# Optimization experiments

Hardware: AMD Instinct MI355X
Metric: run time of the kernel (lower is better)

Reference implementation:

```python
import jax, jax.numpy as jnp
import numpy as np

DIM = 512
HEADS = 8
DIM_HEAD = 32
INNER = HEADS * DIM_HEAD  # 256
B, N = 2, 2048
EPS = 1e-5


def setup_inputs() -> dict:
    key = jax.random.key(0)
    ks = jax.random.split(key, 6)
    x = jax.random.normal(ks[0], (B, N, DIM), dtype=jnp.float32)
    rel_pos_bias = jax.random.normal(ks[1], (HEADS, N, N), dtype=jnp.float32)
    ln_scale = jnp.ones((DIM,), dtype=jnp.float32)
    w_qkv = jax.random.normal(ks[2], (DIM, INNER * 3), dtype=jnp.float32) / np.sqrt(DIM)
    w_out = jax.random.normal(ks[3], (INNER, DIM), dtype=jnp.float32) / np.sqrt(INNER)
    b_out = jnp.zeros((DIM,), dtype=jnp.float32)
    return {"x": x, "rel_pos_bias": rel_pos_bias, "ln_scale": ln_scale,
            "w_qkv": w_qkv, "w_out": w_out, "b_out": b_out}


def reference(x, rel_pos_bias, ln_scale, w_qkv, w_out, b_out):
    scale = DIM_HEAD ** -0.5
    # LayerNorm (no bias), eps=1e-5
    mu = jnp.mean(x, axis=-1, keepdims=True)
    var = jnp.mean(jnp.square(x - mu), axis=-1, keepdims=True)
    xn = (x - mu) * jax.lax.rsqrt(var + EPS) * ln_scale
    # fused QKV projection, no bias
    qkv = xn @ w_qkv  # [b, n, 3*inner]
    q, k, v = jnp.split(qkv, 3, axis=-1)
    def to_heads(t):
        b, n, _ = t.shape
        return t.reshape(b, n, HEADS, DIM_HEAD).transpose(0, 2, 1, 3)  # b h n d
    q, k, v = map(to_heads, (q, k, v))
    q = q * scale
    sim = jnp.einsum('bhid,bhjd->bhij', q, k)
    sim = sim + rel_pos_bias  # (h,n,n) broadcasts over batch
    attn = jax.nn.softmax(sim, axis=-1)
    o = jnp.einsum('bhij,bhjd->bhid', attn, v)
    o = o.transpose(0, 2, 1, 3).reshape(x.shape[0], x.shape[1], INNER)  # b n (h d)
    return o @ w_out + b_out
```

## Files before the change

### kernel.cpp

```cpp
#include <hip/hip_runtime.h>
#include <hip/hip_bf16.h>
#include <cstdint>

#define NB 2
#define NSEQ 2048
#define NDIM 512
#define NHEAD 8
#define DHEAD 32
#define NINNER 256
#define NQKV 768
#define LNEPS 1e-5f
#define QSCALE 0.17677669529663687f

typedef short short8 __attribute__((ext_vector_type(8)));
typedef float f32x4 __attribute__((ext_vector_type(4)));
typedef unsigned short u16;
typedef unsigned int u32;

__device__ __forceinline__ f32x4 mfma16(short8 a, short8 b, f32x4 c) {
    return __builtin_amdgcn_mfma_f32_16x16x32_bf16(a, b, c, 0, 0, 0);
}

__device__ __forceinline__ u16 f2bf(float a) {
    union { float f; u32 u; } x; x.f = a;
    u32 r = x.u + 0x7fffu + ((x.u >> 16) & 1u);
    return (u16)(r >> 16);
}
__device__ __forceinline__ float bf2f(u16 h) {
    union { float f; u32 u; } x; x.u = ((u32)h) << 16; return x.f;
}
__device__ __forceinline__ void split2(float a, u16& hi, u16& lo) {
    hi = f2bf(a);
    lo = f2bf(a - bf2f(hi));
}

__global__ __launch_bounds__(256) void ln_kernel(
    const float* __restrict__ x, const float* __restrict__ gamma,
    u32* __restrict__ xn_hi, u32* __restrict__ xn_lo)
{
    const int row = blockIdx.x;
    const int t = threadIdx.x;
    const float2 v = ((const float2*)(x + (size_t)row * NDIM))[t];
    float s1 = v.x + v.y;
    float s2 = v.x * v.x + v.y * v.y;
    #pragma unroll
    for (int off = 32; off >= 1; off >>= 1) {
        s1 += __shfl_down(s1, off);
        s2 += __shfl_down(s2, off);
    }
    __shared__ float a1[4], a2[4];
    if ((t & 63) == 0) { a1[t >> 6] = s1; a2[t >> 6] = s2; }
    __syncthreads();
    const float ts1 = a1[0] + a1[1] + a1[2] + a1[3];
    const float ts2 = a2[0] + a2[1] + a2[2] + a2[3];
    const float mu = ts1 * (1.0f / NDIM);
    const float var = ts2 * (1.0f / NDIM) - mu * mu;
    const float rs = rsqrtf(var + LNEPS);
    const float2 g = ((const float2*)gamma)[t];
    const float xn0 = (v.x - mu) * rs * g.x;
    const float xn1 = (v.y - mu) * rs * g.y;
    u16 h0, l0, h1, l1;
    split2(xn0, h0, l0);
    split2(xn1, h1, l1);
    xn_hi[(size_t)row * (NDIM / 2) + t] = (u32)h0 | ((u32)h1 << 16);
    xn_lo[(size_t)row * (NDIM / 2) + t] = (u32)l0 | ((u32)l1 << 16);
}

__global__ __launch_bounds__(256) void wsplit_kernel(
    const float* __restrict__ w, u16* __restrict__ tT_hi, u16* __restrict__ tT_lo,
    int K, int Ncols)
{
    const int idx = blockIdx.x * 256 + threadIdx.x;
    const int k = idx / Ncols;
    const int n = idx - k * Ncols;
    u16 hh, ll;
    split2(w[idx], hh, ll);
    tT_hi[(size_t)n * K + k] = hh;
    tT_lo[(size_t)n * K + k] = ll;
}

__global__ __launch_bounds__(256, 4) void qkv_kernel(
    const u16* __restrict__ xn_hi, const u16* __restrict__ xn_lo,
    const u16* __restrict__ wT_hi, const u16* __restrict__ wT_lo,
    u16* __restrict__ q_hi, u16* __restrict__ q_lo,
    u16* __restrict__ k_hi, u16* __restrict__ k_lo,
    u16* __restrict__ vt_hi)
{
    const int t = threadIdx.x;
    const int wave = t >> 6, lane = t & 63;
    const int lrow = lane & 15, lquad = lane >> 4;
    const int rowBase = blockIdx.x * 64;
    const int colBase = blockIdx.y * 64;
    const int wm = (wave >> 1) * 32;
    const int wn = (wave & 1) * 32;
    const int kf = lquad * 8;
    const size_t arow0 = (size_t)(rowBase + wm + lrow) * NDIM;
    const size_t arow1 = (size_t)(rowBase + wm + 16 + lrow) * NDIM;
    const size_t brow0 = (size_t)(colBase + wn + lrow) * NDIM;
    const size_t brow1 = (size_t)(colBase + wn + 16 + lrow) * NDIM;
    const f32x4 zero = {0.f, 0.f, 0.f, 0.f};
    f32x4 acc00 = zero, acc01 = zero, acc10 = zero, acc11 = zero;

    for (int k0 = 0; k0 < NDIM; k0 += 32) {
        const short8 a0h = *(const short8*)(xn_hi + arow0 + k0 + kf);
        const short8 a0l = *(const short8*)(xn_lo + arow0 + k0 + kf);
        const short8 a1h = *(const short8*)(xn_hi + arow1 + k0 + kf);
        const short8 a1l = *(const short8*)(xn_lo + arow1 + k0 + kf);
        const short8 b0h = *(const short8*)(wT_hi + brow0 + k0 + kf);
        const short8 b0l = *(const short8*)(wT_lo + brow0 + k0 + kf);
        const short8 b1h = *(const short8*)(wT_hi + brow1 + k0 + kf);
        const short8 b1l = *(const short8*)(wT_lo + brow1 + k0 + kf);
        acc00 = mfma16(a0h, b0h, acc00); acc00 = mfma16(a0h, b0l, acc00); acc00 = mfma16(a0l, b0h, acc00);
        acc01 = mfma16(a0h, b1h, acc01); acc01 = mfma16(a0h, b1l, acc01); acc01 = mfma16(a0l, b1h, acc01);
        acc10 = mfma16(a1h, b0h, acc10); acc10 = mfma16(a1h, b0l, acc10); acc10 = mfma16(a1l, b0h, acc10);
        acc11 = mfma16(a1h, b1h, acc11); acc11 = mfma16(a1h, b1l, acc11); acc11 = mfma16(a1l, b1h, acc11);
    }

    #pragma unroll
    for (int mi = 0; mi < 2; mi++) {
        #pragma unroll
        for (int ni = 0; ni < 2; ni++) {
            f32x4 acc = (mi == 0) ? ((ni == 0) ? acc00 : acc01)
                                  : ((ni == 0) ? acc10 : acc11);
            #pragma unroll
            for (int r = 0; r < 4; r++) {
                const int grow = rowBase + wm + mi * 16 + lquad * 4 + r;
                const int gcol = colBase + wn + ni * 16 + lrow;
                const float v = acc[r];
                const int bidx = grow >> 11;
                const int n = grow & (NSEQ - 1);
                const int sec = gcol >> 8;
                const int idx = gcol & 255;
                const int head = idx >> 5, d = idx & 31;
                const int bh = bidx * NHEAD + head;
                if (sec == 0) {
                    u16 hh, ll;
                    split2(v * QSCALE, hh, ll);
                    const size_t a = ((size_t)bh * NSEQ + n) * DHEAD + d;
                    q_hi[a] = hh; q_lo[a] = ll;
                } else if (sec == 1) {
                    u16 hh, ll;
                    split2(v, hh, ll);
                    const size_t a = ((size_t)bh * NSEQ + n) * DHEAD + d;
                    k_hi[a] = hh; k_lo[a] = ll;
                } else {
                    const size_t a = ((size_t)bh * DHEAD + d) * NSEQ + n;
                    vt_hi[a] = f2bf(v);
                }
            }
        }
    }
}

__global__ __launch_bounds__(256, 6) void attn_kernel(
    const u16* __restrict__ q_hi, const u16* __restrict__ q_lo,
    const u16* __restrict__ k_hi, const u16* __restrict__ k_lo,
    const u16* __restrict__ vt_hi,
    const float* __restrict__ bias,
    u16* __restrict__ o_hi, u16* __restrict__ o_lo)
{
    __shared__ __align__(16) u16 Ph[4][16][40];
    __shared__ __align__(16) float cA[4][64][4];
    __shared__ __align__(16) float cB[4][64][4];
    __shared__ float cl[4][16];
    const int t = threadIdx.x;
    const int wave = t >> 6, lane = t & 63;
    const int lrow = lane & 15, lquad = lane >> 4;
    const int bh = blockIdx.y;
    const int head = bh & (NHEAD - 1);
    const int qb = blockIdx.x * 16;
    const size_t qkbase = (size_t)bh * NSEQ * DHEAD;
    const short8 qh = *(const short8*)(q_hi + qkbase + (size_t)(qb + lrow) * DHEAD + lquad * 8);
    const short8 ql = *(const short8*)(q_lo + qkbase + (size_t)(qb + lrow) * DHEAD + lquad * 8);
    const f32x4 zero = {0.f, 0.f, 0.f, 0.f};
    f32x4 accA = zero, accB = zero;
    float lp[4] = {0.f, 0.f, 0.f, 0.f};
    const float* biasrow = bias + (size_t)head * NSEQ * NSEQ + (size_t)(qb + lquad * 4) * NSEQ + lrow;
    const size_t vbase = (size_t)bh * DHEAD * NSEQ;
    const int ktbase = wave * 512;

    for (int i = 0; i < 16; i++) {
        const int kt = ktbase + i * 32;
        const short8 kh0 = *(const short8*)(k_hi + qkbase + (size_t)(kt + lrow) * DHEAD + lquad * 8);
        const short8 kl0 = *(const short8*)(k_lo + qkbase + (size_t)(kt + lrow) * DHEAD + lquad * 8);
        const short8 kh1 = *(const short8*)(k_hi + qkbase + (size_t)(kt + 16 + lrow) * DHEAD + lquad * 8);
        const short8 kl1 = *(const short8*)(k_lo + qkbase + (size_t)(kt + 16 + lrow) * DHEAD + lquad * 8);
        f32x4 s0 = zero, s1 = zero;
        s0 = mfma16(qh, kh0, s0); s0 = mfma16(qh, kl0, s0); s0 = mfma16(ql, kh0, s0);
        s1 = mfma16(qh, kh1, s1); s1 = mfma16(qh, kl1, s1); s1 = mfma16(ql, kh1, s1);
        #pragma unroll
        for (int r = 0; r < 4; r++) {
            const float p0 = __expf(s0[r] + biasrow[(size_t)r * NSEQ + kt]);
            const float p1 = __expf(s1[r] + biasrow[(size_t)r * NSEQ + kt + 16]);
            lp[r] += p0 + p1;
            Ph[wave][lquad * 4 + r][lrow] = f2bf(p0);
            Ph[wave][lquad * 4 + r][16 + lrow] = f2bf(p1);
        }
        const short8 ph = *(const short8*)&Ph[wave][lrow][lquad * 8];
        const short8 v0h = *(const short8*)(vt_hi + vbase + (size_t)lrow * NSEQ + kt + lquad * 8);
        const short8 v1h = *(const short8*)(vt_hi + vbase + (size_t)(16 + lrow) * NSEQ + kt + lquad * 8);
        accA = mfma16(ph, v0h, accA);
        accB = mfma16(ph, v1h, accB);
    }

    #pragma unroll
    for (int r = 0; r < 4; r++) {
        lp[r] += __shfl_xor(lp[r], 8);
        lp[r] += __shfl_xor(lp[r], 4);
        lp[r] += __shfl_xor(lp[r], 2);
        lp[r] += __shfl_xor(lp[r], 1);
    }
    *(f32x4*)&cA[wave][lane][0] = accA;
    *(f32x4*)&cB[wave][lane][0] = accB;
    if (lrow == 0) {
        #pragma unroll
        for (int r = 0; r < 4; r++) cl[wave][lquad * 4 + r] = lp[r];
    }
    __syncthreads();
    if (wave == 0) {
        f32x4 sA = *(const f32x4*)&cA[0][lane][0];
        f32x4 sB = *(const f32x4*)&cB[0][lane][0];
        #pragma unroll
        for (int w = 1; w < 4; w++) {
            sA += *(const f32x4*)&cA[w][lane][0];
            sB += *(const f32x4*)&cB[w][lane][0];
        }
        const int bidx = bh >> 3;
        #pragma unroll
        for (int r = 0; r < 4; r++) {
            const float lt = cl[0][lquad * 4 + r] + cl[1][lquad * 4 + r]
                           + cl[2][lquad * 4 + r] + cl[3][lquad * 4 + r];
            const float inv = 1.0f / lt;
            const int q = qb + lquad * 4 + r;
            const size_t base = ((size_t)bidx * NSEQ + q) * NINNER + head * DHEAD;
            u16 hh, ll;
            split2(sA[r] * inv, hh, ll);
            o_hi[base + lrow] = hh; o_lo[base + lrow] = ll;
            split2(sB[r] * inv, hh, ll);
            o_hi[base + 16 + lrow] = hh; o_lo[base + 16 + lrow] = ll;
        }
    }
}

__global__ __launch_bounds__(256, 4) void out_kernel(
    const u16* __restrict__ o_hi, const u16* __restrict__ o_lo,
    const u16* __restrict__ wT_hi, const u16* __restrict__ wT_lo,
    const float* __restrict__ b_out,
    float* __restrict__ out)
{
    const int t = threadIdx.x;
    const int wave = t >> 6, lane = t & 63;
    const int lrow = lane & 15, lquad = lane >> 4;
    const int rowBase = blockIdx.x * 64;
    const int colBase = blockIdx.y * 64;
    const int wm = (wave >> 1) * 32;
    const int wn = (wave & 1) * 32;
    const int kf = lquad * 8;
    const size_t arow0 = (size_t)(rowBase + wm + lrow) * NINNER;
    const size_t arow1 = (size_t)(rowBase + wm + 16 + lrow) * NINNER;
    const size_t brow0 = (size_t)(colBase + wn + lrow) * NINNER;
    const size_t brow1 = (size_t)(colBase + wn + 16 + lrow) * NINNER;
    const f32x4 zero = {0.f, 0.f, 0.f, 0.f};
    f32x4 acc00 = zero, acc01 = zero, acc10 = zero, acc11 = zero;

    for (int k0 = 0; k0 < NINNER; k0 += 32) {
        const short8 a0h = *(const short8*)(o_hi + arow0 + k0 + kf);
        const short8 a0l = *(const short8*)(o_lo + arow0 + k0 + kf);
        const short8 a1h = *(const short8*)(o_hi + arow1 + k0 + kf);
        const short8 a1l = *(const short8*)(o_lo + arow1 + k0 + kf);
        const short8 b0h = *(const short8*)(wT_hi + brow0 + k0 + kf);
        const short8 b0l = *(const short8*)(wT_lo + brow0 + k0 + kf);
        const short8 b1h = *(const short8*)(wT_hi + brow1 + k0 + kf);
        const short8 b1l = *(const short8*)(wT_lo + brow1 + k0 + kf);
        acc00 = mfma16(a0h, b0h, acc00); acc00 = mfma16(a0h, b0l, acc00); acc00 = mfma16(a0l, b0h, acc00);
        acc01 = mfma16(a0h, b1h, acc01); acc01 = mfma16(a0h, b1l, acc01); acc01 = mfma16(a0l, b1h, acc01);
        acc10 = mfma16(a1h, b0h, acc10); acc10 = mfma16(a1h, b0l, acc10); acc10 = mfma16(a1l, b0h, acc10);
        acc11 = mfma16(a1h, b1h, acc11); acc11 = mfma16(a1h, b1l, acc11); acc11 = mfma16(a1l, b1h, acc11);
    }

    #pragma unroll
    for (int mi = 0; mi < 2; mi++) {
        #pragma unroll
        for (int ni = 0; ni < 2; ni++) {
            f32x4 acc = (mi == 0) ? ((ni == 0) ? acc00 : acc01)
                                  : ((ni == 0) ? acc10 : acc11);
            #pragma unroll
            for (int r = 0; r < 4; r++) {
                const int grow = rowBase + wm + mi * 16 + lquad * 4 + r;
                const int gcol = colBase + wn + ni * 16 + lrow;
                out[(size_t)grow * NDIM + gcol] = acc[r] + b_out[gcol];
            }
        }
    }
}

extern "C" void kernel_launch(void* const* d_in, const int* in_sizes, int n_in,
                              void* d_out, int out_size, void* d_ws, size_t ws_size,
                              hipStream_t stream)
{
    (void)in_sizes; (void)n_in; (void)out_size; (void)ws_size;
    const float* x     = (const float*)d_in[0];
    const float* bias  = (const float*)d_in[1];
    const float* gamma = (const float*)d_in[2];
    const float* wqkv  = (const float*)d_in[3];
    const float* wout  = (const float*)d_in[4];
    const float* bout  = (const float*)d_in[5];
    float* out = (float*)d_out;

    char* ws = (char*)d_ws;
    size_t off = 0;
    auto carve = [&](size_t bytes) -> void* {
        void* p = (void*)(ws + off);
        off += (bytes + 255) & ~(size_t)255;
        return p;
    };
    const size_t rows = (size_t)NB * NSEQ;
    const size_t hn = (size_t)NB * NHEAD * NSEQ * DHEAD;
    u16* xn_hi = (u16*)carve(rows * NDIM * 2);
    u16* xn_lo = (u16*)carve(rows * NDIM * 2);
    u16* wqT_hi = (u16*)carve((size_t)NQKV * NDIM * 2);
    u16* wqT_lo = (u16*)carve((size_t)NQKV * NDIM * 2);
    u16* woT_hi = (u16*)carve((size_t)NDIM * NINNER * 2);
    u16* woT_lo = (u16*)carve((size_t)NDIM * NINNER * 2);
    u16* q_hi  = (u16*)carve(hn * 2);
    u16* q_lo  = (u16*)carve(hn * 2);
    u16* k_hi  = (u16*)carve(hn * 2);
    u16* k_lo  = (u16*)carve(hn * 2);
    u16* vt_hi = (u16*)carve(hn * 2);
    u16* o_hi  = (u16*)carve(rows * NINNER * 2);
    u16* o_lo  = (u16*)carve(rows * NINNER * 2);

    ln_kernel<<<dim3((unsigned)rows), 256, 0, stream>>>(x, gamma, (u32*)xn_hi, (u32*)xn_lo);
    wsplit_kernel<<<dim3((NDIM * NQKV) / 256), 256, 0, stream>>>(wqkv, wqT_hi, wqT_lo, NDIM, NQKV);
    wsplit_kernel<<<dim3((NINNER * NDIM) / 256), 256, 0, stream>>>(wout, woT_hi, woT_lo, NINNER, NDIM);
    qkv_kernel<<<dim3(64, 12), 256, 0, stream>>>(xn_hi, xn_lo, wqT_hi, wqT_lo,
                                                 q_hi, q_lo, k_hi, k_lo, vt_hi);
    attn_kernel<<<dim3(128, 16), 256, 0, stream>>>(q_hi, q_lo, k_hi, k_lo,
                                                   vt_hi, bias, o_hi, o_lo);
    out_kernel<<<dim3(64, 8), 256, 0, stream>>>(o_hi, o_lo, woT_hi, woT_lo, bout, out);
}
```

Measured before the change: 342.6 us.

## Share bias across batches in attention, stage GEMM tiles in LDS, tile transposes

The attention kernel now handles both batch items for a head in one block, so each rel_pos_bias tile is loaded once and used for both. Scores are computed transposed (K·Q), and P is passed to the PV MFMA through lane shuffles instead of an LDS round-trip. The QKV and output GEMMs stage A/B tiles in shared memory with smaller row tiles. The weight split/transpose and the V transpose are now separate LDS-tiled kernels with coalesced stores. The added kernel launch, higher register pressure in attention and extra LDS syncs in the GEMMs may offset part of the savings on bias bandwidth, which dominates the cost.

```diff
diff --git a/kernel.cpp b/kernel.cpp
--- a/kernel.cpp
+++ b/kernel.cpp
@@ -14,6 +14,8 @@
 
 typedef short short8 __attribute__((ext_vector_type(8)));
 typedef float f32x4 __attribute__((ext_vector_type(4)));
+typedef unsigned int u32x4 __attribute__((ext_vector_type(4)));
+typedef unsigned int u32x2 __attribute__((ext_vector_type(2)));
 typedef unsigned short u16;
 typedef unsigned int u32;
 
@@ -32,6 +34,9 @@
 __device__ __forceinline__ void split2(float a, u16& hi, u16& lo) {
     hi = f2bf(a);
     lo = f2bf(a - bf2f(hi));
+}
+__device__ __forceinline__ u32 pk2(float a, float b) {
+    return (u32)f2bf(a) | ((u32)f2bf(b) << 16);
 }
 
 __global__ __launch_bounds__(256) void ln_kernel(
@@ -57,26 +62,69 @@
     const float var = ts2 * (1.0f / NDIM) - mu * mu;
     const float rs = rsqrtf(var + LNEPS);
     const float2 g = ((const float2*)gamma)[t];
-    const float xn0 = (v.x - mu) * rs * g.x;
-    const float xn1 = (v.y - mu) * rs * g.y;
     u16 h0, l0, h1, l1;
-    split2(xn0, h0, l0);
-    split2(xn1, h1, l1);
+    split2((v.x - mu) * rs * g.x, h0, l0);
+    split2((v.y - mu) * rs * g.y, h1, l1);
     xn_hi[(size_t)row * (NDIM / 2) + t] = (u32)h0 | ((u32)h1 << 16);
     xn_lo[(size_t)row * (NDIM / 2) + t] = (u32)l0 | ((u32)l1 << 16);
 }
 
-__global__ __launch_bounds__(256) void wsplit_kernel(
-    const float* __restrict__ w, u16* __restrict__ tT_hi, u16* __restrict__ tT_lo,
-    int K, int Ncols)
-{
-    const int idx = blockIdx.x * 256 + threadIdx.x;
-    const int k = idx / Ncols;
-    const int n = idx - k * Ncols;
-    u16 hh, ll;
-    split2(w[idx], hh, ll);
-    tT_hi[(size_t)n * K + k] = hh;
-    tT_lo[(size_t)n * K + k] = ll;
+__global__ __launch_bounds__(256) void wtrans_kernel(
+    const float* __restrict__ w, u16* __restrict__ wT_hi, u16* __restrict__ wT_lo,
+    int K, int N)
+{
+    __shared__ __align__(16) u16 th[64][72], tl[64][72];
+    const int t = threadIdx.x;
+    const int k0 = blockIdx.x * 64, n0 = blockIdx.y * 64;
+    {
+        const int k = t >> 2, c = (t & 3) * 16;
+        const float* src = w + (size_t)(k0 + k) * N + n0 + c;
+        #pragma unroll
+        for (int jj = 0; jj < 4; jj++) {
+            const f32x4 w4 = *(const f32x4*)(src + jj * 4);
+            #pragma unroll
+            for (int e = 0; e < 4; e++) {
+                u16 hh, ll;
+                split2(w4[e], hh, ll);
+                th[k][c + jj * 4 + e] = hh;
+                tl[k][c + jj * 4 + e] = ll;
+            }
+        }
+    }
+    __syncthreads();
+    {
+        const int n = t >> 2, kc = (t & 3) * 16;
+        u16 hb[16], lb[16];
+        #pragma unroll
+        for (int j = 0; j < 16; j++) { hb[j] = th[kc + j][n]; lb[j] = tl[kc + j][n]; }
+        u16* dh = wT_hi + (size_t)(n0 + n) * K + k0 + kc;
+        u16* dl = wT_lo + (size_t)(n0 + n) * K + k0 + kc;
+        *(short8*)dh = *(short8*)hb;
+        *(short8*)(dh + 8) = *(short8*)(hb + 8);
+        *(short8*)dl = *(short8*)lb;
+        *(short8*)(dl + 8) = *(short8*)(lb + 8);
+    }
+}
+
+__global__ __launch_bounds__(256) void vtrans_kernel(
+    const u16* __restrict__ v, u16* __restrict__ vt)
+{
+    __shared__ __align__(16) u16 sh[64][40];
+    const int t = threadIdx.x;
+    const int n0 = blockIdx.x * 64;
+    const int bh = blockIdx.y;
+    {
+        const int n = t >> 2, c = (t & 3) * 8;
+        *(short8*)&sh[n][c] = *(const short8*)(v + ((size_t)bh * NSEQ + n0 + n) * DHEAD + c);
+    }
+    __syncthreads();
+    {
+        const int d = t >> 3, nc = (t & 7) * 8;
+        u16 buf[8];
+        #pragma unroll
+        for (int j = 0; j < 8; j++) buf[j] = sh[nc + j][d];
+        *(short8*)(vt + ((size_t)bh * DHEAD + d) * NSEQ + n0 + nc) = *(short8*)buf;
+    }
 }
 
 __global__ __launch_bounds__(256, 4) void qkv_kernel(
@@ -84,161 +132,208 @@
     const u16* __restrict__ wT_hi, const u16* __restrict__ wT_lo,
     u16* __restrict__ q_hi, u16* __restrict__ q_lo,
     u16* __restrict__ k_hi, u16* __restrict__ k_lo,
-    u16* __restrict__ vt_hi)
-{
+    u16* __restrict__ v)
+{
+    __shared__ __align__(16) u16 Ah[32][40], Al[32][40], Bh[64][40], Bl[64][40];
     const int t = threadIdx.x;
     const int wave = t >> 6, lane = t & 63;
     const int lrow = lane & 15, lquad = lane >> 4;
-    const int rowBase = blockIdx.x * 64;
+    const int rowBase = blockIdx.x * 32;
     const int colBase = blockIdx.y * 64;
-    const int wm = (wave >> 1) * 32;
-    const int wn = (wave & 1) * 32;
+    const int wm = (wave & 1) * 16;
+    const int wn = (wave >> 1) * 32;
     const int kf = lquad * 8;
-    const size_t arow0 = (size_t)(rowBase + wm + lrow) * NDIM;
-    const size_t arow1 = (size_t)(rowBase + wm + 16 + lrow) * NDIM;
-    const size_t brow0 = (size_t)(colBase + wn + lrow) * NDIM;
-    const size_t brow1 = (size_t)(colBase + wn + 16 + lrow) * NDIM;
     const f32x4 zero = {0.f, 0.f, 0.f, 0.f};
-    f32x4 acc00 = zero, acc01 = zero, acc10 = zero, acc11 = zero;
+    f32x4 acc0 = zero, acc1 = zero;
+
+    const int tar = (t & 127) >> 2, tac = ((t & 127) & 3) * 8;
+    const int tbr = t >> 2, tbc = (t & 3) * 8;
 
     for (int k0 = 0; k0 < NDIM; k0 += 32) {
-        const short8 a0h = *(const short8*)(xn_hi + arow0 + k0 + kf);
-        const short8 a0l = *(const short8*)(xn_lo + arow0 + k0 + kf);
-        const short8 a1h = *(const short8*)(xn_hi + arow1 + k0 + kf);
-        const short8 a1l = *(const short8*)(xn_lo + arow1 + k0 + kf);
-        const short8 b0h = *(const short8*)(wT_hi + brow0 + k0 + kf);
-        const short8 b0l = *(const short8*)(wT_lo + brow0 + k0 + kf);
-        const short8 b1h = *(const short8*)(wT_hi + brow1 + k0 + kf);
-        const short8 b1l = *(const short8*)(wT_lo + brow1 + k0 + kf);
-        acc00 = mfma16(a0h, b0h, acc00); acc00 = mfma16(a0h, b0l, acc00); acc00 = mfma16(a0l, b0h, acc00);
-        acc01 = mfma16(a0h, b1h, acc01); acc01 = mfma16(a0h, b1l, acc01); acc01 = mfma16(a0l, b1h, acc01);
-        acc10 = mfma16(a1h, b0h, acc10); acc10 = mfma16(a1h, b0l, acc10); acc10 = mfma16(a1l, b0h, acc10);
-        acc11 = mfma16(a1h, b1h, acc11); acc11 = mfma16(a1h, b1l, acc11); acc11 = mfma16(a1l, b1h, acc11);
+        __syncthreads();
+        if (t < 128)
+            *(short8*)&Ah[tar][tac] = *(const short8*)(xn_hi + (size_t)(rowBase + tar) * NDIM + k0 + tac);
+        else
+            *(short8*)&Al[tar][tac] = *(const short8*)(xn_lo + (size_t)(rowBase + tar) * NDIM + k0 + tac);
+        *(short8*)&Bh[tbr][tbc] = *(const short8*)(wT_hi + (size_t)(colBase + tbr) * NDIM + k0 + tbc);
+        *(short8*)&Bl[tbr][tbc] = *(const short8*)(wT_lo + (size_t)(colBase + tbr) * NDIM + k0 + tbc);
+        __syncthreads();
+        const short8 ah = *(const short8*)&Ah[wm + lrow][kf];
+        const short8 al = *(const short8*)&Al[wm + lrow][kf];
+        const short8 b0h = *(const short8*)&Bh[wn + lrow][kf];
+        const short8 b0l = *(const short8*)&Bl[wn + lrow][kf];
+        const short8 b1h = *(const short8*)&Bh[wn + 16 + lrow][kf];
+        const short8 b1l = *(const short8*)&Bl[wn + 16 + lrow][kf];
+        acc0 = mfma16(ah, b0h, acc0); acc0 = mfma16(ah, b0l, acc0); acc0 = mfma16(al, b0h, acc0);
+        acc1 = mfma16(ah, b1h, acc1); acc1 = mfma16(ah, b1l, acc1); acc1 = mfma16(al, b1h, acc1);
     }
 
     #pragma unroll
-    for (int mi = 0; mi < 2; mi++) {
-        #pragma unroll
-        for (int ni = 0; ni < 2; ni++) {
-            f32x4 acc = (mi == 0) ? ((ni == 0) ? acc00 : acc01)
-                                  : ((ni == 0) ? acc10 : acc11);
+    for (int ni = 0; ni < 2; ni++) {
+        const f32x4 acc = ni ? acc1 : acc0;
+        #pragma unroll
+        for (int r = 0; r < 4; r++) {
+            const int grow = rowBase + wm + lquad * 4 + r;
+            const int gcol = colBase + wn + ni * 16 + lrow;
+            const float val = acc[r];
+            const int bidx = grow >> 11;
+            const int n = grow & (NSEQ - 1);
+            const int sec = gcol >> 8;
+            const int idx = gcol & 255;
+            const int head = idx >> 5, d = idx & 31;
+            const int bh = bidx * NHEAD + head;
+            if (sec == 0) {
+                u16 hh, ll;
+                split2(val * QSCALE, hh, ll);
+                const size_t a = ((size_t)bh * NSEQ + n) * DHEAD + d;
+                q_hi[a] = hh; q_lo[a] = ll;
+            } else if (sec == 1) {
+                u16 hh, ll;
+                split2(val, hh, ll);
+                const size_t a = ((size_t)bh * NSEQ + n) * DHEAD + d;
+                k_hi[a] = hh; k_lo[a] = ll;
+            } else {
+                v[((size_t)bh * NSEQ + n) * DHEAD + d] = f2bf(val);
+            }
+        }
+    }
+}
+
+__global__ __launch_bounds__(256, 4) void attn_kernel(
+    const u16* __restrict__ q_hi, const u16* __restrict__ q_lo,
+    const u16* __restrict__ k_hi, const u16* __restrict__ k_lo,
+    const u16* __restrict__ vt,
+    const float* __restrict__ bias,
+    u16* __restrict__ o_hi, u16* __restrict__ o_lo)
+{
+    __shared__ __align__(16) float cA[2][4][64][4];
+    __shared__ __align__(16) float cB[2][4][64][4];
+    __shared__ float cl[2][4][16];
+    const int t = threadIdx.x;
+    const int wave = t >> 6, lane = t & 63;
+    const int lrow = lane & 15, lquad = lane >> 4;
+    const int head = blockIdx.y;
+    const int qb = blockIdx.x * 16;
+    const size_t qk0 = (size_t)head * NSEQ * DHEAD;
+    const size_t qk1 = (size_t)(NHEAD + head) * NSEQ * DHEAD;
+    const size_t qoff = (size_t)(qb + lrow) * DHEAD + lquad * 8;
+    const short8 qh0 = *(const short8*)(q_hi + qk0 + qoff);
+    const short8 ql0 = *(const short8*)(q_lo + qk0 + qoff);
+    const short8 qh1 = *(const short8*)(q_hi + qk1 + qoff);
+    const short8 ql1 = *(const short8*)(q_lo + qk1 + qoff);
+    const f32x4 zero = {0.f, 0.f, 0.f, 0.f};
+    f32x4 accA0 = zero, accB0 = zero, accA1 = zero, accB1 = zero;
+    float lp0 = 0.f, lp1 = 0.f;
+    const float* bptr = bias + (size_t)head * NSEQ * NSEQ + (size_t)(qb + lrow) * NSEQ;
+    const int kt0 = wave * 512;
+    const int src1 = lrow | (((2 * lquad) & 3) << 4);
+    const int src2 = lrow | (((2 * lquad + 1) & 3) << 4);
+    const bool qtop = lquad < 2;
+
+    for (int i = 0; i < 16; i++) {
+        const int kt = kt0 + i * 32;
+        const size_t koff = (size_t)(kt + lrow) * DHEAD + lquad * 8;
+        const short8 ka0h = *(const short8*)(k_hi + qk0 + koff);
+        const short8 ka0l = *(const short8*)(k_lo + qk0 + koff);
+        const short8 ka1h = *(const short8*)(k_hi + qk0 + koff + 16 * DHEAD);
+        const short8 ka1l = *(const short8*)(k_lo + qk0 + koff + 16 * DHEAD);
+        const short8 kb0h = *(const short8*)(k_hi + qk1 + koff);
+        const short8 kb0l = *(const short8*)(k_lo + qk1 + koff);
+        const short8 kb1h = *(const short8*)(k_hi + qk1 + koff + 16 * DHEAD);
+        const short8 kb1l = *(const short8*)(k_lo + qk1 + koff + 16 * DHEAD);
+        const short8 va0 = *(const short8*)(vt + qk0 + (size_t)lrow * NSEQ + kt + lquad * 8);
+        const short8 va1 = *(const short8*)(vt + qk0 + (size_t)(16 + lrow) * NSEQ + kt + lquad * 8);
+        const short8 vb0 = *(const short8*)(vt + qk1 + (size_t)lrow * NSEQ + kt + lquad * 8);
+        const short8 vb1 = *(const short8*)(vt + qk1 + (size_t)(16 + lrow) * NSEQ + kt + lquad * 8);
+        const f32x4 bias0 = *(const f32x4*)(bptr + kt + lquad * 4);
+        const f32x4 bias1 = *(const f32x4*)(bptr + kt + 16 + lquad * 4);
+
+        {
+            f32x4 c0 = zero, c1 = zero;
+            c0 = mfma16(ka0h, qh0, c0); c0 = mfma16(ka0h, ql0, c0); c0 = mfma16(ka0l, qh0, c0);
+            c1 = mfma16(ka1h, qh0, c1); c1 = mfma16(ka1h, ql0, c1); c1 = mfma16(ka1l, qh0, c1);
+            f32x4 p0, p1;
             #pragma unroll
             for (int r = 0; r < 4; r++) {
-                const int grow = rowBase + wm + mi * 16 + lquad * 4 + r;
-                const int gcol = colBase + wn + ni * 16 + lrow;
-                const float v = acc[r];
-                const int bidx = grow >> 11;
-                const int n = grow & (NSEQ - 1);
-                const int sec = gcol >> 8;
-                const int idx = gcol & 255;
-                const int head = idx >> 5, d = idx & 31;
-                const int bh = bidx * NHEAD + head;
-                if (sec == 0) {
-                    u16 hh, ll;
-                    split2(v * QSCALE, hh, ll);
-                    const size_t a = ((size_t)bh * NSEQ + n) * DHEAD + d;
-                    q_hi[a] = hh; q_lo[a] = ll;
-                } else if (sec == 1) {
-                    u16 hh, ll;
-                    split2(v, hh, ll);
-                    const size_t a = ((size_t)bh * NSEQ + n) * DHEAD + d;
-                    k_hi[a] = hh; k_lo[a] = ll;
-                } else {
-                    const size_t a = ((size_t)bh * DHEAD + d) * NSEQ + n;
-                    vt_hi[a] = f2bf(v);
-                }
+                p0[r] = __expf(c0[r] + bias0[r]);
+                p1[r] = __expf(c1[r] + bias1[r]);
             }
-        }
-    }
-}
-
-__global__ __launch_bounds__(256, 6) void attn_kernel(
-    const u16* __restrict__ q_hi, const u16* __restrict__ q_lo,
-    const u16* __restrict__ k_hi, const u16* __restrict__ k_lo,
-    const u16* __restrict__ vt_hi,
-    const float* __restrict__ bias,
-    u16* __restrict__ o_hi, u16* __restrict__ o_lo)
-{
-    __shared__ __align__(16) u16 Ph[4][16][40];
-    __shared__ __align__(16) float cA[4][64][4];
-    __shared__ __align__(16) float cB[4][64][4];
-    __shared__ float cl[4][16];
-    const int t = threadIdx.x;
-    const int wave = t >> 6, lane = t & 63;
-    const int lrow = lane & 15, lquad = lane >> 4;
-    const int bh = blockIdx.y;
-    const int head = bh & (NHEAD - 1);
-    const int qb = blockIdx.x * 16;
-    const size_t qkbase = (size_t)bh * NSEQ * DHEAD;
-    const short8 qh = *(const short8*)(q_hi + qkbase + (size_t)(qb + lrow) * DHEAD + lquad * 8);
-    const short8 ql = *(const short8*)(q_lo + qkbase + (size_t)(qb + lrow) * DHEAD + lquad * 8);
-    const f32x4 zero = {0.f, 0.f, 0.f, 0.f};
-    f32x4 accA = zero, accB = zero;
-    float lp[4] = {0.f, 0.f, 0.f, 0.f};
-    const float* biasrow = bias + (size_t)head * NSEQ * NSEQ + (size_t)(qb + lquad * 4) * NSEQ + lrow;
-    const size_t vbase = (size_t)bh * DHEAD * NSEQ;
-    const int ktbase = wave * 512;
-
-    for (int i = 0; i < 16; i++) {
-        const int kt = ktbase + i * 32;
-        const short8 kh0 = *(const short8*)(k_hi + qkbase + (size_t)(kt + lrow) * DHEAD + lquad * 8);
-        const short8 kl0 = *(const short8*)(k_lo + qkbase + (size_t)(kt + lrow) * DHEAD + lquad * 8);
-        const short8 kh1 = *(const short8*)(k_hi + qkbase + (size_t)(kt + 16 + lrow) * DHEAD + lquad * 8);
-        const short8 kl1 = *(const short8*)(k_lo + qkbase + (size_t)(kt + 16 + lrow) * DHEAD + lquad * 8);
-        f32x4 s0 = zero, s1 = zero;
-        s0 = mfma16(qh, kh0, s0); s0 = mfma16(qh, kl0, s0); s0 = mfma16(ql, kh0, s0);
-        s1 = mfma16(qh, kh1, s1); s1 = mfma16(qh, kl1, s1); s1 = mfma16(ql, kh1, s1);
+            lp0 += (p0[0] + p0[1]) + (p0[2] + p0[3]) + (p1[0] + p1[1]) + (p1[2] + p1[3]);
+            const u32 a0 = pk2(p0[0], p0[1]), a1 = pk2(p0[2], p0[3]);
+            const u32 b0 = pk2(p1[0], p1[1]), b1 = pk2(p1[2], p1[3]);
+            const u32 s1a0 = (u32)__shfl((int)a0, src1), s1a1 = (u32)__shfl((int)a1, src1);
+            const u32 s1b0 = (u32)__shfl((int)b0, src1), s1b1 = (u32)__shfl((int)b1, src1);
+            const u32 s2a0 = (u32)__shfl((int)a0, src2), s2a1 = (u32)__shfl((int)a1, src2);
+            const u32 s2b0 = (u32)__shfl((int)b0, src2), s2b1 = (u32)__shfl((int)b1, src2);
+            union { u32x4 u; short8 s; } cv;
+            cv.u[0] = qtop ? s1a0 : s1b0;
+            cv.u[1] = qtop ? s1a1 : s1b1;
+            cv.u[2] = qtop ? s2a0 : s2b0;
+            cv.u[3] = qtop ? s2a1 : s2b1;
+            accA0 = mfma16(va0, cv.s, accA0);
+            accB0 = mfma16(va1, cv.s, accB0);
+        }
+        {
+            f32x4 c0 = zero, c1 = zero;
+            c0 = mfma16(kb0h, qh1, c0); c0 = mfma16(kb0h, ql1, c0); c0 = mfma16(kb0l, qh1, c0);
+            c1 = mfma16(kb1h, qh1, c1); c1 = mfma16(kb1h, ql1, c1); c1 = mfma16(kb1l, qh1, c1);
+            f32x4 p0, p1;
+            #pragma unroll
+            for (int r = 0; r < 4; r++) {
+                p0[r] = __expf(c0[r] + bias0[r]);
+                p1[r] = __expf(c1[r] + bias1[r]);
+            }
+            lp1 += (p0[0] + p0[1]) + (p0[2] + p0[3]) + (p1[0] + p1[1]) + (p1[2] + p1[3]);
+            const u32 a0 = pk2(p0[0], p0[1]), a1 = pk2(p0[2], p0[3]);
+            const u32 b0 = pk2(p1[0], p1[1]), b1 = pk2(p1[2], p1[3]);
+            const u32 s1a0 = (u32)__shfl((int)a0, src1), s1a1 = (u32)__shfl((int)a1, src1);
+            const u32 s1b0 = (u32)__shfl((int)b0, src1), s1b1 = (u32)__shfl((int)b1, src1);
+            const u32 s2a0 = (u32)__shfl((int)a0, src2), s2a1 = (u32)__shfl((int)a1, src2);
+            const u32 s2b0 = (u32)__shfl((int)b0, src2), s2b1 = (u32)__shfl((int)b1, src2);
+            union { u32x4 u; short8 s; } cv;
+            cv.u[0] = qtop ? s1a0 : s1b0;
+            cv.u[1] = qtop ? s1a1 : s1b1;
+            cv.u[2] = qtop ? s2a0 : s2b0;
+            cv.u[3] = qtop ? s2a1 : s2b1;
+            accA1 = mfma16(vb0, cv.s, accA1);
+            accB1 = mfma16(vb1, cv.s, accB1);
+        }
+    }
+
+    lp0 += __shfl_xor(lp0, 16); lp0 += __shfl_xor(lp0, 32);
+    lp1 += __shfl_xor(lp1, 16); lp1 += __shfl_xor(lp1, 32);
+
+    *(f32x4*)&cA[0][wave][lane][0] = accA0;
+    *(f32x4*)&cB[0][wave][lane][0] = accB0;
+    *(f32x4*)&cA[1][wave][lane][0] = accA1;
+    *(f32x4*)&cB[1][wave][lane][0] = accB1;
+    if (lquad == 0) {
+        cl[0][wave][lrow] = lp0;
+        cl[1][wave][lrow] = lp1;
+    }
+    __syncthreads();
+    if (wave < 2) {
+        const int b = wave;
+        f32x4 sA = *(const f32x4*)&cA[b][0][lane][0];
+        f32x4 sB = *(const f32x4*)&cB[b][0][lane][0];
+        #pragma unroll
+        for (int w = 1; w < 4; w++) {
+            sA += *(const f32x4*)&cA[b][w][lane][0];
+            sB += *(const f32x4*)&cB[b][w][lane][0];
+        }
+        const float lt = cl[b][0][lrow] + cl[b][1][lrow] + cl[b][2][lrow] + cl[b][3][lrow];
+        const float inv = 1.0f / lt;
+        const size_t base = ((size_t)b * NSEQ + qb + lrow) * NINNER + head * DHEAD + lquad * 4;
+        u16 h[8], l[8];
         #pragma unroll
         for (int r = 0; r < 4; r++) {
-            const float p0 = __expf(s0[r] + biasrow[(size_t)r * NSEQ + kt]);
-            const float p1 = __expf(s1[r] + biasrow[(size_t)r * NSEQ + kt + 16]);
-            lp[r] += p0 + p1;
-            Ph[wave][lquad * 4 + r][lrow] = f2bf(p0);
-            Ph[wave][lquad * 4 + r][16 + lrow] = f2bf(p1);
-        }
-        const short8 ph = *(const short8*)&Ph[wave][lrow][lquad * 8];
-        const short8 v0h = *(const short8*)(vt_hi + vbase + (size_t)lrow * NSEQ + kt + lquad * 8);
-        const short8 v1h = *(const short8*)(vt_hi + vbase + (size_t)(16 + lrow) * NSEQ + kt + lquad * 8);
-        accA = mfma16(ph, v0h, accA);
-        accB = mfma16(ph, v1h, accB);
-    }
-
-    #pragma unroll
-    for (int r = 0; r < 4; r++) {
-        lp[r] += __shfl_xor(lp[r], 8);
-        lp[r] += __shfl_xor(lp[r], 4);
-        lp[r] += __shfl_xor(lp[r], 2);
-        lp[r] += __shfl_xor(lp[r], 1);
-    }
-    *(f32x4*)&cA[wave][lane][0] = accA;
-    *(f32x4*)&cB[wave][lane][0] = accB;
-    if (lrow == 0) {
-        #pragma unroll
-        for (int r = 0; r < 4; r++) cl[wave][lquad * 4 + r] = lp[r];
-    }
-    __syncthreads();
-    if (wave == 0) {
-        f32x4 sA = *(const f32x4*)&cA[0][lane][0];
-        f32x4 sB = *(const f32x4*)&cB[0][lane][0];
-        #pragma unroll
-        for (int w = 1; w < 4; w++) {
-            sA += *(const f32x4*)&cA[w][lane][0];
-            sB += *(const f32x4*)&cB[w][lane][0];
-        }
-        const int bidx = bh >> 3;
-        #pragma unroll
-        for (int r = 0; r < 4; r++) {
-            const float lt = cl[0][lquad * 4 + r] + cl[1][lquad * 4 + r]
-                           + cl[2][lquad * 4 + r] + cl[3][lquad * 4 + r];
-            const float inv = 1.0f / lt;
-            const int q = qb + lquad * 4 + r;
-            const size_t base = ((size_t)bidx * NSEQ + q) * NINNER + head * DHEAD;
-            u16 hh, ll;
-            split2(sA[r] * inv, hh, ll);
-            o_hi[base + lrow] = hh; o_lo[base + lrow] = ll;
-            split2(sB[r] * inv, hh, ll);
-            o_hi[base + 16 + lrow] = hh; o_lo[base + 16 + lrow] = ll;
-        }
+            split2(sA[r] * inv, h[r], l[r]);
+            split2(sB[r] * inv, h[4 + r], l[4 + r]);
+        }
+        *(u32x2*)&o_hi[base] = *(u32x2*)&h[0];
+        *(u32x2*)&o_hi[base + 16] = *(u32x2*)&h[4];
+        *(u32x2*)&o_lo[base] = *(u32x2*)&l[0];
+        *(u32x2*)&o_lo[base + 16] = *(u32x2*)&l[4];
     }
 }
 
@@ -248,48 +343,48 @@
     const float* __restrict__ b_out,
     float* __restrict__ out)
 {
+    __shared__ __align__(16) u16 Ah[32][40], Al[32][40], Bh[64][40], Bl[64][40];
     const int t = threadIdx.x;
     const int wave = t >> 6, lane = t & 63;
     const int lrow = lane & 15, lquad = lane >> 4;
-    const int rowBase = blockIdx.x * 64;
+    const int rowBase = blockIdx.x * 32;
     const int colBase = blockIdx.y * 64;
-    const int wm = (wave >> 1) * 32;
-    const int wn = (wave & 1) * 32;
+    const int wm = (wave & 1) * 16;
+    const int wn = (wave >> 1) * 32;
     const int kf = lquad * 8;
-    const size_t arow0 = (size_t)(rowBase + wm + lrow) * NINNER;
-    const size_t arow1 = (size_t)(rowBase + wm + 16 + lrow) * NINNER;
-    const size_t brow0 = (size_t)(colBase + wn + lrow) * NINNER;
-    const size_t brow1 = (size_t)(colBase + wn + 16 + lrow) * NINNER;
     const f32x4 zero = {0.f, 0.f, 0.f, 0.f};
-    f32x4 acc00 = zero, acc01 = zero, acc10 = zero, acc11 = zero;
+    f32x4 acc0 = zero, acc1 = zero;
+
+    const int tar = (t & 127) >> 2, tac = ((t & 127) & 3) * 8;
+    const int tbr = t >> 2, tbc = (t & 3) * 8;
 
     for (int k0 = 0; k0 < NINNER; k0 += 32) {
-        const short8 a0h = *(const short8*)(o_hi + arow0 + k0 + kf);
-        const short8 a0l = *(const short8*)(o_lo + arow0 + k0 + kf);
-        const short8 a1h = *(const short8*)(o_hi + arow1 + k0 + kf);
-        const short8 a1l = *(const short8*)(o_lo + arow1 + k0 + kf);
-        const short8 b0h = *(const short8*)(wT_hi + brow0 + k0 + kf);
-        const short8 b0l = *(const short8*)(wT_lo + brow0 + k0 + kf);
-        const short8 b1h = *(const short8*)(wT_hi + brow1 + k0 + kf);
-        const short8 b1l = *(const short8*)(wT_lo + brow1 + k0 + kf);
-        acc00 = mfma16(a0h, b0h, acc00); acc00 = mfma16(a0h, b0l, acc00); acc00 = mfma16(a0l, b0h, acc00);
-        acc01 = mfma16(a0h, b1h, acc01); acc01 = mfma16(a0h, b1l, acc01); acc01 = mfma16(a0l, b1h, acc01);
-        acc10 = mfma16(a1h, b0h, acc10); acc10 = mfma16(a1h, b0l, acc10); acc10 = mfma16(a1l, b0h, acc10);
-        acc11 = mfma16(a1h, b1h, acc11); acc11 = mfma16(a1h, b1l, acc11); acc11 = mfma16(a1l, b1h, acc11);
+        __syncthreads();
+        if (t < 128)
+            *(short8*)&Ah[tar][tac] = *(const short8*)(o_hi + (size_t)(rowBase + tar) * NINNER + k0 + tac);
+        else
+            *(short8*)&Al[tar][tac] = *(const short8*)(o_lo + (size_t)(rowBase + tar) * NINNER + k0 + tac);
+        *(short8*)&Bh[tbr][tbc] = *(const short8*)(wT_hi + (size_t)(colBase + tbr) * NINNER + k0 + tbc);
+        *(short8*)&Bl[tbr][tbc] = *(const short8*)(wT_lo + (size_t)(colBase + tbr) * NINNER + k0 + tbc);
+        __syncthreads();
+        const short8 ah = *(const short8*)&Ah[wm + lrow][kf];
+        const short8 al = *(const short8*)&Al[wm + lrow][kf];
+        const short8 b0h = *(const short8*)&Bh[wn + lrow][kf];
+        const short8 b0l = *(const short8*)&Bl[wn + lrow][kf];
+        const short8 b1h = *(const short8*)&Bh[wn + 16 + lrow][kf];
+        const short8 b1l = *(const short8*)&Bl[wn + 16 + lrow][kf];
+        acc0 = mfma16(ah, b0h, acc0); acc0 = mfma16(ah, b0l, acc0); acc0 = mfma16(al, b0h, acc0);
+        acc1 = mfma16(ah, b1h, acc1); acc1 = mfma16(ah, b1l, acc1); acc1 = mfma16(al, b1h, acc1);
     }
 
     #pragma unroll
-    for (int mi = 0; mi < 2; mi++) {
-        #pragma unroll
-        for (int ni = 0; ni < 2; ni++) {
-            f32x4 acc = (mi == 0) ? ((ni == 0) ? acc00 : acc01)
-                                  : ((ni == 0) ? acc10 : acc11);
-            #pragma unroll
-            for (int r = 0; r < 4; r++) {
-                const int grow = rowBase + wm + mi * 16 + lquad * 4 + r;
-                const int gcol = colBase + wn + ni * 16 + lrow;
-                out[(size_t)grow * NDIM + gcol] = acc[r] + b_out[gcol];
-            }
+    for (int ni = 0; ni < 2; ni++) {
+        const f32x4 acc = ni ? acc1 : acc0;
+        #pragma unroll
+        for (int r = 0; r < 4; r++) {
+            const int grow = rowBase + wm + lquad * 4 + r;
+            const int gcol = colBase + wn + ni * 16 + lrow;
+            out[(size_t)grow * NDIM + gcol] = acc[r] + b_out[gcol];
         }
     }
 }
@@ -326,16 +421,18 @@
     u16* q_lo  = (u16*)carve(hn * 2);
     u16* k_hi  = (u16*)carve(hn * 2);
     u16* k_lo  = (u16*)carve(hn * 2);
-    u16* vt_hi = (u16*)carve(hn * 2);
+    u16* vbuf  = (u16*)carve(hn * 2);
+    u16* vt    = (u16*)carve(hn * 2);
     u16* o_hi  = (u16*)carve(rows * NINNER * 2);
     u16* o_lo  = (u16*)carve(rows * NINNER * 2);
 
     ln_kernel<<<dim3((unsigned)rows), 256, 0, stream>>>(x, gamma, (u32*)xn_hi, (u32*)xn_lo);
-    wsplit_kernel<<<dim3((NDIM * NQKV) / 256), 256, 0, stream>>>(wqkv, wqT_hi, wqT_lo, NDIM, NQKV);
-    wsplit_kernel<<<dim3((NINNER * NDIM) / 256), 256, 0, stream>>>(wout, woT_hi, woT_lo, NINNER, NDIM);
-    qkv_kernel<<<dim3(64, 12), 256, 0, stream>>>(xn_hi, xn_lo, wqT_hi, wqT_lo,
-                                                 q_hi, q_lo, k_hi, k_lo, vt_hi);
-    attn_kernel<<<dim3(128, 16), 256, 0, stream>>>(q_hi, q_lo, k_hi, k_lo,
-                                                   vt_hi, bias, o_hi, o_lo);
-    out_kernel<<<dim3(64, 8), 256, 0, stream>>>(o_hi, o_lo, woT_hi, woT_lo, bout, out);
-}
+    wtrans_kernel<<<dim3(NDIM / 64, NQKV / 64), 256, 0, stream>>>(wqkv, wqT_hi, wqT_lo, NDIM, NQKV);
+    wtrans_kernel<<<dim3(NINNER / 64, NDIM / 64), 256, 0, stream>>>(wout, woT_hi, woT_lo, NINNER, NDIM);
+    qkv_kernel<<<dim3(128, 12), 256, 0, stream>>>(xn_hi, xn_lo, wqT_hi, wqT_lo,
+                                                  q_hi, q_lo, k_hi, k_lo, vbuf);
+    vtrans_kernel<<<dim3(NSEQ / 64, NB * NHEAD), 256, 0, stream>>>(vbuf, vt);
+    attn_kernel<<<dim3(128, 8), 256, 0, stream>>>(q_hi, q_lo, k_hi, k_lo,
+                                                  vt, bias, o_hi, o_lo);
+    out_kernel<<<dim3(128, 8), 256, 0, stream>>>(o_hi, o_lo, woT_hi, woT_lo, bout, out);
+}
```

After: 308.6 us. -9.9%, faster.
